# Performance work log

Measured on AMD Instinct MI355X. Metric: run time of the kernel, lower is better.

Reference implementation:

```python
import jax, jax.numpy as jnp
import numpy as np

HIDDEN_DIM = 32
EDGE_DIM = 16
EDGE_HIDDEN = 64
N_EDGES = 250000


def setup_inputs() -> dict:
    key = jax.random.key(0)
    k1, k2, k3, k4, k5 = jax.random.split(key, 5)
    h_v = jax.random.normal(k1, (N_EDGES, HIDDEN_DIM), dtype=jnp.float32)
    h_w = jax.random.normal(k2, (N_EDGES, HIDDEN_DIM), dtype=jnp.float32)
    edge_features = jax.random.normal(k3, (N_EDGES, EDGE_DIM), dtype=jnp.float32)
    # Edge-network MLP params: edge_dim -> edge_hidden -> hidden_dim^2
    W1 = jax.random.normal(k4, (EDGE_DIM, EDGE_HIDDEN), dtype=jnp.float32) * (1.0 / np.sqrt(EDGE_DIM))
    b1 = jnp.zeros((EDGE_HIDDEN,), dtype=jnp.float32)
    W2 = jax.random.normal(k5, (EDGE_HIDDEN, HIDDEN_DIM * HIDDEN_DIM), dtype=jnp.float32) * (1.0 / np.sqrt(EDGE_HIDDEN))
    b2 = jnp.zeros((HIDDEN_DIM * HIDDEN_DIM,), dtype=jnp.float32)
    return {"h_v": h_v, "h_w": h_w, "edge_features": edge_features,
            "W1": W1, "b1": b1, "W2": W2, "b2": b2}


def reference(h_v, h_w, edge_features, W1, b1, W2, b2):
    # 1. Edge MLP: (n_edges, edge_dim) -> (n_edges, d*d)
    hdn = jax.nn.relu(edge_features @ W1 + b1)          # (E, edge_hidden)
    A = (hdn @ W2 + b2)                                  # (E, d*d)
    # 2. Reshape to per-edge matrices (E, d, d)
    d = h_w.shape[-1]
    A = A.reshape(-1, d, d)
    # 3. Per-edge matrix-vector product: M = A(e_vw) @ h_w
    messages = jnp.einsum('eij,ej->ei', A, h_w)          # (E, d)
    return messages
```

## Files before the change

### kernel.cpp

```cpp
#include <hip/hip_runtime.h>

typedef unsigned short u16;
typedef _Float16 f16x2 __attribute__((ext_vector_type(2)));
typedef _Float16 f16x8 __attribute__((ext_vector_type(8)));
typedef float    f32x4  __attribute__((ext_vector_type(4)));
typedef float    f32x16 __attribute__((ext_vector_type(16)));


union U4 { uint4 u; f16x8 h; u16 s[8]; };
union HU { f16x2 h2[4]; f16x8 h8; };

__global__ void prep_kernel(const float* __restrict__ W1,
                            const float* __restrict__ b1,
                            const float* __restrict__ W2,
                            const float* __restrict__ b2,
                            u16* __restrict__ ws)
{
    int id = blockIdx.x * 256 + threadIdx.x;
    if (id < 8320) {
        int k2 = id >> 6, l = id & 63;
        int h = l >> 5, col = l & 31;
        U4 o;
        #pragma unroll
        for (int g = 0; g < 2; ++g) {
            int base4 = k2 * 16 + g * 8 + h * 4;
            f32x4 v;
            if (base4 < 2048) {
                int k1 = base4 >> 5, j32 = base4 & 31;
                v = *(const f32x4*)&W2[k1 * 1024 + col * 32 + j32];
            } else {
                v = *(const f32x4*)&b2[col * 32 + (base4 - 2048)];
            }
            #pragma unroll
            for (int j = 0; j < 4; ++j)
                o.h[g * 4 + j] = (_Float16)v[j];
        }
        *(uint4*)(ws + id * 8) = o.u;
    } else if (id < 8448) {
        int idx = id - 8320;
        int nt = idx >> 6, l = idx & 63;
        int h = l >> 5, col = nt * 32 + (l & 31);
        U4 o;
        #pragma unroll
        for (int g = 0; g < 2; ++g)
            #pragma unroll
            for (int j = 0; j < 4; ++j) {
                int k = g * 8 + h * 4 + j;
                o.h[g * 4 + j] = (_Float16)W1[k * 64 + col];
            }
        *(uint4*)(ws + id * 8) = o.u;
    } else if (id < 8512) {
        int idx = id - 8448;
        int hh = idx >> 5, nt = (idx >> 4) & 1, r = idx & 15;
        int row = (r & 3) + 8 * (r >> 2) + 4 * hh;
        ((float*)(ws + 67584))[idx] = b1[nt * 32 + row];
    }
}

__device__ __forceinline__ void stage16(const void* g, void* l) {
    __builtin_amdgcn_global_load_lds(
        (const __attribute__((address_space(1))) void*)g,
        (__attribute__((address_space(3))) void*)l, 16, 0, 0);
}

__global__ __launch_bounds__(256, 3) void edge_kernel(
    const float* __restrict__ h_w,
    const float* __restrict__ ef,
    const u16*  __restrict__ ws,
    float* __restrict__ out,
    int E)
{
    __shared__ alignas(16) u16 shm[16384];
    const int tid  = threadIdx.x;
    const int lane = tid & 63;
    const int l31  = lane & 31;
    const int h    = lane >> 5;
    const int tileBase = (blockIdx.x * 4 + (tid >> 6)) * 64;
    const char* wsb = (const char*)ws;
    char*       shb = (char*)shm;

    #pragma unroll
    for (int j = 0; j < 4; ++j)
        stage16(wsb + j * 4096 + tid * 16, shb + j * 4096 + tid * 16);

    f16x2 hwA[2][2][4];
    #pragma unroll
    for (int mt = 0; mt < 2; ++mt) {
        int e = tileBase + mt * 32 + l31;
        bool ok = e < E;
        f32x4 q0 = {}, q1 = {}, q2 = {}, q3 = {};
        if (ok) {
            const float* hp = h_w + (size_t)e * 32 + h * 4;
            q0 = *(const f32x4*)(hp);
            q1 = *(const f32x4*)(hp + 8);
            q2 = *(const f32x4*)(hp + 16);
            q3 = *(const f32x4*)(hp + 24);
        }
        hwA[mt][0][0] = f16x2{ (_Float16)q0[0], (_Float16)q0[1] };
        hwA[mt][0][1] = f16x2{ (_Float16)q0[2], (_Float16)q0[3] };
        hwA[mt][0][2] = f16x2{ (_Float16)q1[0], (_Float16)q1[1] };
        hwA[mt][0][3] = f16x2{ (_Float16)q1[2], (_Float16)q1[3] };
        hwA[mt][1][0] = f16x2{ (_Float16)q2[0], (_Float16)q2[1] };
        hwA[mt][1][1] = f16x2{ (_Float16)q2[2], (_Float16)q2[3] };
        hwA[mt][1][2] = f16x2{ (_Float16)q3[0], (_Float16)q3[1] };
        hwA[mt][1][3] = f16x2{ (_Float16)q3[2], (_Float16)q3[3] };
    }

    const uint4* W1f = (const uint4*)(ws + 8320 * 8);
    U4 w1f0, w1f1;
    w1f0.u = W1f[lane];
    w1f1.u = W1f[64 + lane];
    const float* b1pf = (const float*)(ws + 67584);
    f32x4 bv[2][4];
    #pragma unroll
    for (int nt = 0; nt < 2; ++nt)
        #pragma unroll
        for (int qr = 0; qr < 4; ++qr)
            bv[nt][qr] = *(const f32x4*)(b1pf + h * 32 + nt * 16 + qr * 4);

    f16x2 Q[2][2][8][2];
    #pragma unroll
    for (int mt = 0; mt < 2; ++mt) {
        int e = tileBase + mt * 32 + l31;
        bool ok = e < E;
        f32x4 g0 = {}, g1 = {};
        if (ok) {
            g0 = *(const f32x4*)&ef[e * 16 + h * 4];
            g1 = *(const f32x4*)&ef[e * 16 + 8 + h * 4];
        }
        U4 a;
        #pragma unroll
        for (int j = 0; j < 4; ++j) {
            a.h[j]     = (_Float16)g0[j];
            a.h[4 + j] = (_Float16)g1[j];
        }
        f32x16 c0 = {}, c1 = {};
        c0 = __builtin_amdgcn_mfma_f32_32x32x16_f16(w1f0.h, a.h, c0, 0, 0, 0);
        c1 = __builtin_amdgcn_mfma_f32_32x32x16_f16(w1f1.h, a.h, c1, 0, 0, 0);
        #pragma unroll
        for (int nt = 0; nt < 2; ++nt) {
            #pragma unroll
            for (int p = 0; p < 8; ++p) {
                float r0 = (nt ? c1[2 * p]     : c0[2 * p]);
                float r1 = (nt ? c1[2 * p + 1] : c0[2 * p + 1]);
                float v0 = fmaxf(r0 + bv[nt][p >> 1][(2 * p) & 3],     0.f);
                float v1 = fmaxf(r1 + bv[nt][p >> 1][(2 * p + 1) & 3], 0.f);
                f16x2 own = { (_Float16)v0, (_Float16)v1 };
                unsigned swu = __shfl_xor(__builtin_bit_cast(unsigned, own), 32, 64);
                f16x2 sw = __builtin_bit_cast(f16x2, swu);
                Q[mt][nt][p][0] = h ? sw : own;
                Q[mt][nt][p][1] = h ? own : sw;
            }
        }
    }

    f32x16 accA[2] = {}, accB[2] = {};
    __syncthreads();

    #pragma unroll
    for (int c = 0; c < 8; ++c) {
        if (c < 7) {
            #pragma unroll
            for (int j = 0; j < 4; ++j)
                stage16(wsb + (c + 1) * 16384 + j * 4096 + tid * 16,
                        shb + ((c + 1) & 1) * 16384 + j * 4096 + tid * 16);
        } else {
            if (tid < 128)
                stage16(wsb + 131072 + tid * 16, shb + tid * 16);
        }
        const char* bB = shb + (c & 1) * 16384;
        #pragma unroll
        for (int qq = 0; qq < 8; ++qq) {
            const int k1   = c * 8 + qq;
            const int nt   = k1 >> 5;
            const int q    = k1 & 31;
            const int pa   = ((q & 3) >> 1) + 2 * (q >> 3);
            const int half = q & 1;
            const int hq   = (q >> 2) & 1;
            U4 bf0, bf1;
            bf0.u = *(const uint4*)(bB + (2 * qq) * 1024 + lane * 16);
            bf1.u = *(const uint4*)(bB + (2 * qq + 1) * 1024 + lane * 16);
            _Float16 x0 = Q[0][nt][pa][hq][half];
            _Float16 x1 = Q[1][nt][pa][hq][half];
            f16x2 hh0 = { x0, x0 }, hh1 = { x1, x1 };
            HU A0, A1;
            #pragma unroll
            for (int rr = 0; rr < 4; ++rr) { A0.h2[rr] = hh0 * hwA[0][0][rr]; A1.h2[rr] = hh1 * hwA[1][0][rr]; }
            if (qq & 1) {
                accB[0] = __builtin_amdgcn_mfma_f32_32x32x16_f16(A0.h8, bf0.h, accB[0], 0, 0, 0);
                accB[1] = __builtin_amdgcn_mfma_f32_32x32x16_f16(A1.h8, bf0.h, accB[1], 0, 0, 0);
            } else {
                accA[0] = __builtin_amdgcn_mfma_f32_32x32x16_f16(A0.h8, bf0.h, accA[0], 0, 0, 0);
                accA[1] = __builtin_amdgcn_mfma_f32_32x32x16_f16(A1.h8, bf0.h, accA[1], 0, 0, 0);
            }
            #pragma unroll
            for (int rr = 0; rr < 4; ++rr) { A0.h2[rr] = hh0 * hwA[0][1][rr]; A1.h2[rr] = hh1 * hwA[1][1][rr]; }
            if (qq & 1) {
                accB[0] = __builtin_amdgcn_mfma_f32_32x32x16_f16(A0.h8, bf1.h, accB[0], 0, 0, 0);
                accB[1] = __builtin_amdgcn_mfma_f32_32x32x16_f16(A1.h8, bf1.h, accB[1], 0, 0, 0);
            } else {
                accA[0] = __builtin_amdgcn_mfma_f32_32x32x16_f16(A0.h8, bf1.h, accA[0], 0, 0, 0);
                accA[1] = __builtin_amdgcn_mfma_f32_32x32x16_f16(A1.h8, bf1.h, accA[1], 0, 0, 0);
            }
        }
        __syncthreads();
    }

    {
        U4 bf0, bf1;
        bf0.u = *(const uint4*)(shb + lane * 16);
        bf1.u = *(const uint4*)(shb + 1024 + lane * 16);
        HU A0, A1;
        #pragma unroll
        for (int rr = 0; rr < 4; ++rr) { A0.h2[rr] = hwA[0][0][rr]; A1.h2[rr] = hwA[1][0][rr]; }
        accA[0] = __builtin_amdgcn_mfma_f32_32x32x16_f16(A0.h8, bf0.h, accA[0], 0, 0, 0);
        accA[1] = __builtin_amdgcn_mfma_f32_32x32x16_f16(A1.h8, bf0.h, accA[1], 0, 0, 0);
        #pragma unroll
        for (int rr = 0; rr < 4; ++rr) { A0.h2[rr] = hwA[0][1][rr]; A1.h2[rr] = hwA[1][1][rr]; }
        accA[0] = __builtin_amdgcn_mfma_f32_32x32x16_f16(A0.h8, bf1.h, accA[0], 0, 0, 0);
        accA[1] = __builtin_amdgcn_mfma_f32_32x32x16_f16(A1.h8, bf1.h, accA[1], 0, 0, 0);
    }

    #pragma unroll
    for (int mt = 0; mt < 2; ++mt) {
        #pragma unroll
        for (int r = 0; r < 16; ++r) {
            int row = (r & 3) + 8 * (r >> 2) + 4 * h;
            int e = tileBase + mt * 32 + row;
            if (e < E) out[(size_t)e * 32 + l31] = accA[mt][r] + accB[mt][r];
        }
    }
}

extern "C" void kernel_launch(void* const* d_in, const int* in_sizes, int n_in,
                              void* d_out, int out_size, void* d_ws, size_t ws_size,
                              hipStream_t stream)
{
    const float* h_w = (const float*)d_in[1];
    const float* ef  = (const float*)d_in[2];
    const float* W1  = (const float*)d_in[3];
    const float* b1  = (const float*)d_in[4];
    const float* W2  = (const float*)d_in[5];
    const float* b2  = (const float*)d_in[6];
    float* out = (float*)d_out;
    const int E = in_sizes[1] / 32;
    u16* ws = (u16*)d_ws;

    prep_kernel<<<34, 256, 0, stream>>>(W1, b1, W2, b2, ws);

    const int blocks = (E + 255) / 256;
    edge_kernel<<<blocks, 256, 0, stream>>>(h_w, ef, ws, out, E);
}
```

Measured before the change: 47.81 us.

## Triple-buffer W2 staging in LDS with explicit vmcnt waits and raw barriers

Switches the W2 fragment staging from double to triple buffering in LDS, prefetching two chunks ahead. Full __syncthreads are replaced by targeted s_waitcnt vmcnt plus s_barrier, so outstanding async loads are not drained early. The bias chunk is folded into a padded ninth iteration, and MFMA issue is wrapped in s_setprio. The cost is more LDS per block (48KB vs 32KB), which may limit occupancy, and the hand-counted vmcnt values are fragile.

Result: slower. 51.91 us (+8.6%).

```diff
diff --git a/kernel.cpp b/kernel.cpp
--- a/kernel.cpp
+++ b/kernel.cpp
@@ -17,28 +17,32 @@
                             u16* __restrict__ ws)
 {
     int id = blockIdx.x * 256 + threadIdx.x;
-    if (id < 8320) {
+    if (id < 8704) {
         int k2 = id >> 6, l = id & 63;
         int h = l >> 5, col = l & 31;
         U4 o;
-        #pragma unroll
-        for (int g = 0; g < 2; ++g) {
-            int base4 = k2 * 16 + g * 8 + h * 4;
-            f32x4 v;
-            if (base4 < 2048) {
-                int k1 = base4 >> 5, j32 = base4 & 31;
-                v = *(const f32x4*)&W2[k1 * 1024 + col * 32 + j32];
-            } else {
-                v = *(const f32x4*)&b2[col * 32 + (base4 - 2048)];
-            }
-            #pragma unroll
-            for (int j = 0; j < 4; ++j)
-                o.h[g * 4 + j] = (_Float16)v[j];
+        if (k2 < 130) {
+            #pragma unroll
+            for (int g = 0; g < 2; ++g) {
+                int base4 = k2 * 16 + g * 8 + h * 4;
+                f32x4 v;
+                if (base4 < 2048) {
+                    int k1 = base4 >> 5, j32 = base4 & 31;
+                    v = *(const f32x4*)&W2[k1 * 1024 + col * 32 + j32];
+                } else {
+                    v = *(const f32x4*)&b2[col * 32 + (base4 - 2048)];
+                }
+                #pragma unroll
+                for (int j = 0; j < 4; ++j)
+                    o.h[g * 4 + j] = (_Float16)v[j];
+            }
+        } else {
+            o.u = uint4{0u, 0u, 0u, 0u};
         }
         *(uint4*)(ws + id * 8) = o.u;
-    } else if (id < 8448) {
-        int idx = id - 8320;
-        int nt = idx >> 6, l = idx & 63;
+    } else if (id < 8832) {
+        int idx = id - 8704;
+        int nt = (idx >> 6) & 1, l = idx & 63;
         int h = l >> 5, col = nt * 32 + (l & 31);
         U4 o;
         #pragma unroll
@@ -48,12 +52,12 @@
                 int k = g * 8 + h * 4 + j;
                 o.h[g * 4 + j] = (_Float16)W1[k * 64 + col];
             }
-        *(uint4*)(ws + id * 8) = o.u;
-    } else if (id < 8512) {
-        int idx = id - 8448;
+        *(uint4*)(ws + 69632 + idx * 8) = o.u;
+    } else if (id < 8896) {
+        int idx = id - 8832;
         int hh = idx >> 5, nt = (idx >> 4) & 1, r = idx & 15;
         int row = (r & 3) + 8 * (r >> 2) + 4 * hh;
-        ((float*)(ws + 67584))[idx] = b1[nt * 32 + row];
+        ((float*)(ws + 71680))[idx] = b1[nt * 32 + row];
     }
 }
 
@@ -70,10 +74,10 @@
     float* __restrict__ out,
     int E)
 {
-    __shared__ alignas(16) u16 shm[16384];
+    __shared__ alignas(16) u16 shm[24576];
     const int tid  = threadIdx.x;
     const int lane = tid & 63;
-    const int l31  = lane & 31;
+    const int l31  = lane & 63 & 31;
     const int h    = lane >> 5;
     const int tileBase = (blockIdx.x * 4 + (tid >> 6)) * 64;
     const char* wsb = (const char*)ws;
@@ -82,6 +86,9 @@
     #pragma unroll
     for (int j = 0; j < 4; ++j)
         stage16(wsb + j * 4096 + tid * 16, shb + j * 4096 + tid * 16);
+    #pragma unroll
+    for (int j = 0; j < 4; ++j)
+        stage16(wsb + 16384 + j * 4096 + tid * 16, shb + 16384 + j * 4096 + tid * 16);
 
     f16x2 hwA[2][2][4];
     #pragma unroll
@@ -106,11 +113,11 @@
         hwA[mt][1][3] = f16x2{ (_Float16)q3[2], (_Float16)q3[3] };
     }
 
-    const uint4* W1f = (const uint4*)(ws + 8320 * 8);
+    const uint4* W1f = (const uint4*)(ws + 69632);
     U4 w1f0, w1f1;
     w1f0.u = W1f[lane];
     w1f1.u = W1f[64 + lane];
-    const float* b1pf = (const float*)(ws + 67584);
+    const float* b1pf = (const float*)(ws + 71680);
     f32x4 bv[2][4];
     #pragma unroll
     for (int nt = 0; nt < 2; ++nt)
@@ -155,70 +162,80 @@
     }
 
     f32x16 accA[2] = {}, accB[2] = {};
-    __syncthreads();
-
-    #pragma unroll
-    for (int c = 0; c < 8; ++c) {
-        if (c < 7) {
+
+    asm volatile("s_waitcnt vmcnt(4)" ::: "memory");
+    __builtin_amdgcn_sched_barrier(0);
+    __builtin_amdgcn_s_barrier();
+
+    #pragma unroll
+    for (int c = 0; c < 9; ++c) {
+        if (c + 2 <= 7) {
             #pragma unroll
             for (int j = 0; j < 4; ++j)
-                stage16(wsb + (c + 1) * 16384 + j * 4096 + tid * 16,
-                        shb + ((c + 1) & 1) * 16384 + j * 4096 + tid * 16);
-        } else {
-            if (tid < 128)
-                stage16(wsb + 131072 + tid * 16, shb + tid * 16);
-        }
-        const char* bB = shb + (c & 1) * 16384;
+                stage16(wsb + (c + 2) * 16384 + j * 4096 + tid * 16,
+                        shb + ((c + 2) % 3) * 16384 + j * 4096 + tid * 16);
+        } else if (c + 2 == 8) {
+            #pragma unroll
+            for (int j = 0; j < 2; ++j)
+                stage16(wsb + 131072 + j * 4096 + tid * 16,
+                        shb + (8 % 3) * 16384 + j * 4096 + tid * 16);
+        }
+        const char* bB = shb + (c % 3) * 16384;
+        const int nk = (c < 8) ? 8 : 4;
         #pragma unroll
         for (int qq = 0; qq < 8; ++qq) {
-            const int k1   = c * 8 + qq;
-            const int nt   = k1 >> 5;
-            const int q    = k1 & 31;
-            const int pa   = ((q & 3) >> 1) + 2 * (q >> 3);
-            const int half = q & 1;
-            const int hq   = (q >> 2) & 1;
+            if (qq >= nk) break;
+            const int k1 = c * 8 + qq;
             U4 bf0, bf1;
             bf0.u = *(const uint4*)(bB + (2 * qq) * 1024 + lane * 16);
             bf1.u = *(const uint4*)(bB + (2 * qq + 1) * 1024 + lane * 16);
-            _Float16 x0 = Q[0][nt][pa][hq][half];
-            _Float16 x1 = Q[1][nt][pa][hq][half];
-            f16x2 hh0 = { x0, x0 }, hh1 = { x1, x1 };
-            HU A0, A1;
-            #pragma unroll
-            for (int rr = 0; rr < 4; ++rr) { A0.h2[rr] = hh0 * hwA[0][0][rr]; A1.h2[rr] = hh1 * hwA[1][0][rr]; }
-            if (qq & 1) {
+            HU A0, A1, B0, B1;
+            if (k1 < 64) {
+                const int nt   = k1 >> 5;
+                const int q    = k1 & 31;
+                const int pa   = ((q & 3) >> 1) + 2 * (q >> 3);
+                const int half = q & 1;
+                const int hq   = (q >> 2) & 1;
+                _Float16 x0 = Q[0][nt][pa][hq][half];
+                _Float16 x1 = Q[1][nt][pa][hq][half];
+                f16x2 hh0 = { x0, x0 }, hh1 = { x1, x1 };
+                #pragma unroll
+                for (int rr = 0; rr < 4; ++rr) {
+                    A0.h2[rr] = hh0 * hwA[0][0][rr];
+                    A1.h2[rr] = hh1 * hwA[1][0][rr];
+                    B0.h2[rr] = hh0 * hwA[0][1][rr];
+                    B1.h2[rr] = hh1 * hwA[1][1][rr];
+                }
+            } else {
+                #pragma unroll
+                for (int rr = 0; rr < 4; ++rr) {
+                    A0.h2[rr] = hwA[0][0][rr];
+                    A1.h2[rr] = hwA[1][0][rr];
+                    B0.h2[rr] = hwA[0][1][rr];
+                    B1.h2[rr] = hwA[1][1][rr];
+                }
+            }
+            __builtin_amdgcn_s_setprio(1);
+            if (k1 & 1) {
                 accB[0] = __builtin_amdgcn_mfma_f32_32x32x16_f16(A0.h8, bf0.h, accB[0], 0, 0, 0);
                 accB[1] = __builtin_amdgcn_mfma_f32_32x32x16_f16(A1.h8, bf0.h, accB[1], 0, 0, 0);
+                accB[0] = __builtin_amdgcn_mfma_f32_32x32x16_f16(B0.h8, bf1.h, accB[0], 0, 0, 0);
+                accB[1] = __builtin_amdgcn_mfma_f32_32x32x16_f16(B1.h8, bf1.h, accB[1], 0, 0, 0);
             } else {
                 accA[0] = __builtin_amdgcn_mfma_f32_32x32x16_f16(A0.h8, bf0.h, accA[0], 0, 0, 0);
                 accA[1] = __builtin_amdgcn_mfma_f32_32x32x16_f16(A1.h8, bf0.h, accA[1], 0, 0, 0);
-            }
-            #pragma unroll
-            for (int rr = 0; rr < 4; ++rr) { A0.h2[rr] = hh0 * hwA[0][1][rr]; A1.h2[rr] = hh1 * hwA[1][1][rr]; }
-            if (qq & 1) {
-                accB[0] = __builtin_amdgcn_mfma_f32_32x32x16_f16(A0.h8, bf1.h, accB[0], 0, 0, 0);
-                accB[1] = __builtin_amdgcn_mfma_f32_32x32x16_f16(A1.h8, bf1.h, accB[1], 0, 0, 0);
-            } else {
-                accA[0] = __builtin_amdgcn_mfma_f32_32x32x16_f16(A0.h8, bf1.h, accA[0], 0, 0, 0);
-                accA[1] = __builtin_amdgcn_mfma_f32_32x32x16_f16(A1.h8, bf1.h, accA[1], 0, 0, 0);
-            }
-        }
-        __syncthreads();
-    }
-
-    {
-        U4 bf0, bf1;
-        bf0.u = *(const uint4*)(shb + lane * 16);
-        bf1.u = *(const uint4*)(shb + 1024 + lane * 16);
-        HU A0, A1;
-        #pragma unroll
-        for (int rr = 0; rr < 4; ++rr) { A0.h2[rr] = hwA[0][0][rr]; A1.h2[rr] = hwA[1][0][rr]; }
-        accA[0] = __builtin_amdgcn_mfma_f32_32x32x16_f16(A0.h8, bf0.h, accA[0], 0, 0, 0);
-        accA[1] = __builtin_amdgcn_mfma_f32_32x32x16_f16(A1.h8, bf0.h, accA[1], 0, 0, 0);
-        #pragma unroll
-        for (int rr = 0; rr < 4; ++rr) { A0.h2[rr] = hwA[0][1][rr]; A1.h2[rr] = hwA[1][1][rr]; }
-        accA[0] = __builtin_amdgcn_mfma_f32_32x32x16_f16(A0.h8, bf1.h, accA[0], 0, 0, 0);
-        accA[1] = __builtin_amdgcn_mfma_f32_32x32x16_f16(A1.h8, bf1.h, accA[1], 0, 0, 0);
+                accA[0] = __builtin_amdgcn_mfma_f32_32x32x16_f16(B0.h8, bf1.h, accA[0], 0, 0, 0);
+                accA[1] = __builtin_amdgcn_mfma_f32_32x32x16_f16(B1.h8, bf1.h, accA[1], 0, 0, 0);
+            }
+            __builtin_amdgcn_s_setprio(0);
+        }
+        if (c < 8) {
+            if (c <= 5)      { asm volatile("s_waitcnt vmcnt(4)" ::: "memory"); }
+            else if (c == 6) { asm volatile("s_waitcnt vmcnt(2)" ::: "memory"); }
+            else             { asm volatile("s_waitcnt vmcnt(0)" ::: "memory"); }
+            __builtin_amdgcn_sched_barrier(0);
+            __builtin_amdgcn_s_barrier();
+        }
     }
 
     #pragma unroll
@@ -246,7 +263,7 @@
     const int E = in_sizes[1] / 32;
     u16* ws = (u16*)d_ws;
 
-    prep_kernel<<<34, 256, 0, stream>>>(W1, b1, W2, b2, ws);
+    prep_kernel<<<35, 256, 0, stream>>>(W1, b1, W2, b2, ws);
 
     const int blocks = (E + 255) / 256;
     edge_kernel<<<blocks, 256, 0, stream>>>(h_w, ef, ws, out, E);
```
